# Optimization experiments

Measured on AMD Instinct MI355X. Metric: run time of the kernel, lower is better.

Reference implementation:

```python
import jax, jax.numpy as jnp
import numpy as np

B, T, S = 64, 128, 16
E = 512           # d2v input size
H = 512           # bi-LSTM output size (args.d2v_embed)
Hh = H // 2       # per-direction hidden
NL = 2            # num_layers
ED = 128          # args.embedding_dim
USERS, ARTS, PAD = 100000, 100000, 0


def setup_inputs() -> dict:
    key = jax.random.key(0)
    ks = jax.random.split(key, 32)
    p = 0.02
    inp = {}
    inp["x1"] = jax.random.normal(ks[0], (B, T, E), jnp.float32)
    inp["sample_d2v_embeds"] = jax.random.normal(ks[1], (B, T, S, H), jnp.float32)
    # LSTM params: layer-0 input E == layer-1 input H, so stackable. gate order i,f,g,o
    inp["lstm_Wih"] = jax.random.normal(ks[2], (NL, 2, 4 * Hh, E), jnp.float32) * p
    inp["lstm_Whh"] = jax.random.normal(ks[3], (NL, 2, 4 * Hh, Hh), jnp.float32) * p
    inp["lstm_bih"] = jax.random.normal(ks[4], (NL, 2, 4 * Hh), jnp.float32) * p
    inp["lstm_bhh"] = jax.random.normal(ks[5], (NL, 2, 4 * Hh), jnp.float32) * p
    inp["attn_W1"] = jax.random.normal(ks[6], (H, H), jnp.float32) * p
    inp["attn_b1"] = jax.random.normal(ks[7], (H,), jnp.float32) * p
    inp["attn_w2"] = jax.random.normal(ks[8], (H,), jnp.float32) * p
    inp["rnn_mlp_W"] = jax.random.normal(ks[9], (64, H), jnp.float32) * p
    inp["rnn_mlp_b"] = jax.random.normal(ks[10], (64,), jnp.float32) * p
    inp["user_table"] = jax.random.normal(ks[11], (USERS, ED), jnp.float32) * p
    inp["art_table"] = (jax.random.normal(ks[12], (ARTS, ED), jnp.float32) * p).at[PAD].set(0.0)
    inp["em_W1"] = jax.random.normal(ks[13], (128, ED), jnp.float32) * p
    inp["em_b1"] = jax.random.normal(ks[14], (128,), jnp.float32) * p
    inp["em_W2"] = jax.random.normal(ks[15], (64, 128), jnp.float32) * p
    inp["em_b2"] = jax.random.normal(ks[16], (64,), jnp.float32) * p
    inp["lm_W1"] = jax.random.normal(ks[17], (256, 128), jnp.float32) * p
    inp["lm_b1"] = jax.random.normal(ks[18], (256,), jnp.float32) * p
    inp["lm_W2"] = jax.random.normal(ks[19], (128, 256), jnp.float32) * p
    inp["lm_b2"] = jax.random.normal(ks[20], (128,), jnp.float32) * p
    inp["lm_W3"] = jax.random.normal(ks[21], (64, 128), jnp.float32) * p
    inp["lm_b3"] = jax.random.normal(ks[22], (64,), jnp.float32) * p
    inp["lm_W4"] = jax.random.normal(ks[23], (1, 64), jnp.float32) * p
    inp["lm_b4"] = jax.random.normal(ks[24], (1,), jnp.float32) * p
    inp["x2"] = 0  # unused '_' arg
    inp["cate"] = jax.random.randint(ks[25], (B, T), 0, 10)  # unused by forward
    lens = jax.random.randint(ks[26], (B,), 1, T + 1)
    inp["seq_lens"] = jnp.sort(lens)[::-1]  # pack requires descending
    inp["user_ids"] = jax.random.randint(ks[27], (B,), 0, USERS)
    inp["sample_ids"] = jax.random.randint(ks[28], (B, T, S), 0, ARTS)
    return inp


def _bilstm(x, lens, Wih, Whh, bih, bhh):
    # Packed bidirectional LSTM == padded LSTM with state updates masked to t < len.
    Bc, Tc, _ = x.shape
    tmask = jnp.arange(Tc)[None, :] < lens[:, None]       # [B,T]
    m_t = tmask.T[:, :, None]                             # [T,B,1]
    for l in range(NL):
        outs = []
        for d, rev in ((0, False), (1, True)):
            xg = jnp.einsum('bti,gi->tbg', x, Wih[l, d]) + bih[l, d]  # [T,B,4Hh]
            Whh_ld, bhh_ld = Whh[l, d], bhh[l, d]

            def step(carry, inp_t, Whh_ld=Whh_ld, bhh_ld=bhh_ld):
                h, c = carry
                xg_t, m = inp_t
                g = xg_t + h @ Whh_ld.T + bhh_ld
                i_, f_, g_, o_ = jnp.split(g, 4, axis=-1)
                c2 = jax.nn.sigmoid(f_) * c + jax.nn.sigmoid(i_) * jnp.tanh(g_)
                h2 = jax.nn.sigmoid(o_) * jnp.tanh(c2)
                h = jnp.where(m, h2, h)
                c = jnp.where(m, c2, c)
                return (h, c), h

            init = (jnp.zeros((Bc, Hh), x.dtype), jnp.zeros((Bc, Hh), x.dtype))
            _, hs = jax.lax.scan(step, init, (xg, m_t), reverse=rev)
            outs.append(jnp.transpose(hs, (1, 0, 2)))
        x = jnp.concatenate(outs, axis=-1)                # [B,T,H]
    return x, tmask


def reference(x1, sample_d2v_embeds, lstm_Wih, lstm_Whh, lstm_bih, lstm_bhh,
              attn_W1, attn_b1, attn_w2, rnn_mlp_W, rnn_mlp_b,
              user_table, art_table, em_W1, em_b1, em_W2, em_b2,
              lm_W1, lm_b1, lm_W2, lm_b2, lm_W3, lm_b3, lm_W4, lm_b4,
              x2, cate, seq_lens, user_ids, sample_ids):
    rnn, tmask = _bilstm(x1, seq_lens, lstm_Wih, lstm_Whh, lstm_bih, lstm_bhh)
    # per-key MLP attention score, causal softmax, weighted sum (the packed double loop)
    sc = jnp.einsum('bth,h->bt', jnp.tanh(jnp.einsum('bth,oh->bto', rnn, attn_W1) + attn_b1), attn_w2)
    causal = jnp.tril(jnp.ones((rnn.shape[1], rnn.shape[1]), bool))
    logits = jnp.where(causal[None, :, :], sc[:, None, :], jnp.float32(-1e30))
    a = jax.nn.softmax(logits, axis=-1)                   # [B,T(query),T(key)]
    ctx = jnp.einsum('bts,bsh->bth', a, rnn)
    ctx = jnp.where(tmask[:, :, None], ctx, 0.0)          # rnn_step zeros at padded t
    # embedding branch
    ue = user_table[user_ids]                             # [B,ED]
    se = art_table[sample_ids]                            # [B,T,S,ED]
    e = ue[:, None, None, :] * se
    e = jax.nn.relu(e @ em_W1.T + em_b1)
    e = jax.nn.relu(e @ em_W2.T + em_b2)                  # [B,T,S,64]
    # rnn branch
    r = ctx[:, :, None, :] * sample_d2v_embeds
    r = r @ rnn_mlp_W.T + rnn_mlp_b                       # [B,T,S,64]
    z = jnp.concatenate([e, r], axis=-1)                  # [B,T,S,128]
    z = jax.nn.relu(z @ lm_W1.T + lm_b1)
    z = jax.nn.relu(z @ lm_W2.T + lm_b2)
    z = jax.nn.relu(z @ lm_W3.T + lm_b3)
    z = jax.nn.sigmoid(z @ lm_W4.T + lm_b4)
    return jnp.squeeze(z, axis=-1)                        # [B,T,S]
```

## Files before the change

kernel.cpp:

```cpp
#include <hip/hip_runtime.h>
#include <cstddef>

namespace {

constexpr int T = 128;

typedef unsigned short u16;
typedef unsigned int u32;
typedef __attribute__((ext_vector_type(8))) short short8;
typedef __attribute__((ext_vector_type(4))) float f32x4;
typedef __attribute__((ext_vector_type(4))) int i32x4;

__device__ __forceinline__ u16 f2bf(float x) {
  u32 u = __float_as_uint(x);
  u = (u + 0x7FFFu + ((u >> 16) & 1u)) >> 16;
  return (u16)u;
}
__device__ __forceinline__ float bf2f(u16 v) {
  return __uint_as_float(((u32)v) << 16);
}
__device__ __forceinline__ float sigf(float x) {
  return __builtin_amdgcn_rcpf(1.f + __builtin_amdgcn_exp2f(-1.44269504f * x));
}
__device__ __forceinline__ float tanh2(float x) {
  return 1.f - 2.f * __builtin_amdgcn_rcpf(1.f + __builtin_amdgcn_exp2f(2.88539008f * x));
}
__device__ __forceinline__ void bar_lds() {
  asm volatile("s_waitcnt lgkmcnt(0)\n\ts_barrier" ::: "memory");
}

constexpr int O_WIH = 0;
constexpr int O_AW1 = 2097152;
constexpr int O_EM1 = 2359296;
constexpr int O_EM2 = 2375680;
constexpr int O_MLP = 2383872;
constexpr int O_LW1 = 2416640;
constexpr int O_LW2 = 2449408;
constexpr int O_LW3 = 2482176;
constexpr int N_WBF = 2490368;

__global__ __launch_bounds__(256)
void k_prep(const float* __restrict__ wih, const float* __restrict__ aw1,
            const float* __restrict__ e1, const float* __restrict__ e2,
            const float* __restrict__ mw, const float* __restrict__ l1,
            const float* __restrict__ l2, const float* __restrict__ l3,
            u16* __restrict__ wbf) {
  int i = blockIdx.x * 256 + threadIdx.x;
  if (i >= N_WBF) return;
  float v;
  if (i < O_AW1)      v = wih[i];
  else if (i < O_EM1) v = aw1[i - O_AW1];
  else if (i < O_EM2) v = e1[i - O_EM1];
  else if (i < O_MLP) v = e2[i - O_EM2];
  else if (i < O_LW1) v = mw[i - O_MLP];
  else if (i < O_LW2) v = l1[i - O_LW1];
  else if (i < O_LW3) v = l2[i - O_LW2];
  else                v = l3[i - O_LW3];
  wbf[i] = f2bf(v);
}

__global__ __launch_bounds__(256)
void k_prepw(const float* __restrict__ whh, signed char* __restrict__ wq) {
  int i = blockIdx.x * 256 + threadIdx.x;
  float v = whh[i] * 1016.f;
  v = fminf(fmaxf(v, -127.f), 127.f);
  wq[i] = (signed char)(int)rintf(v);
}

__global__ __launch_bounds__(256)
void k_xg_mfma(const float* __restrict__ X, const u16* __restrict__ Wbf,
               const float* __restrict__ bi, const float* __restrict__ bh,
               float* __restrict__ xg) {
  __shared__ __align__(16) u16 sx[32 * 520];
  int tid = threadIdx.x;
  int rowbase = blockIdx.x * 32;
  int nchunk = blockIdx.y;
  for (int idx = tid; idx < 4096; idx += 256) {
    int r = idx >> 7, k4 = idx & 127;
    float4 v = *(const float4*)(X + (size_t)(rowbase + r) * 512 + k4 * 4);
    u32* p = (u32*)(sx + r * 520 + k4 * 4);
    p[0] = (u32)f2bf(v.x) | ((u32)f2bf(v.y) << 16);
    p[1] = (u32)f2bf(v.z) | ((u32)f2bf(v.w) << 16);
  }
  __syncthreads();
  int w = tid >> 6, lane = tid & 63;
  int msub = w >> 1, nhalf = w & 1;
  int mbase = msub * 16;
  int nb0 = nchunk * 256 + nhalf * 128;
  f32x4 acc[8];
#pragma unroll
  for (int i = 0; i < 8; ++i) acc[i] = f32x4{0.f, 0.f, 0.f, 0.f};
  for (int kt = 0; kt < 16; ++kt) {
    short8 a = *(const short8*)(sx + (mbase + (lane & 15)) * 520 + kt * 32 + (lane >> 4) * 8);
#pragma unroll
    for (int nt = 0; nt < 8; ++nt) {
      short8 b = *(const short8*)(Wbf + (size_t)(nb0 + nt * 16 + (lane & 15)) * 512 +
                                  kt * 32 + (lane >> 4) * 8);
      acc[nt] = __builtin_amdgcn_mfma_f32_16x16x32_bf16(a, b, acc[nt], 0, 0, 0);
    }
  }
  int mr = mbase + (lane >> 4) * 4;
#pragma unroll
  for (int nt = 0; nt < 8; ++nt) {
    int n = nb0 + nt * 16 + (lane & 15);
    float bb = bi[n] + bh[n];
#pragma unroll
    for (int r = 0; r < 4; ++r)
      xg[(size_t)(rowbase + mr + r) * 2048 + n] = acc[nt][r] + bb;
  }
}

__global__ __launch_bounds__(512, 1)
void k_lstm6(const float* __restrict__ xg, const signed char* __restrict__ wq,
             const int* __restrict__ lens, float* __restrict__ out, int layer) {
  __shared__ __align__(16) signed char hq[2][16 * 272];
  const int d = blockIdx.x >> 2, bg = blockIdx.x & 3;
  const int tid = threadIdx.x;
  const int jc = tid >> 6, l = tid & 63, ln = l & 15, lk = l >> 4;
  const int mb = bg * 16;

  i32x4 Bq[4][2][4];
  const signed char* wbase = wq + (size_t)(layer * 2 + d) * 262144;
#pragma unroll
  for (int g = 0; g < 4; ++g)
#pragma unroll
    for (int js = 0; js < 2; ++js)
#pragma unroll
      for (int kc = 0; kc < 4; ++kc) {
        int n = g * 256 + jc * 32 + js * 16 + ln;
        Bq[g][js][kc] = *(const i32x4*)(wbase + (size_t)n * 256 + kc * 64 + lk * 16);
      }

  int mlen[4];
#pragma unroll
  for (int r = 0; r < 4; ++r) mlen[r] = lens[mb + lk * 4 + r];

  float cst[2][4], hst[2][4];
#pragma unroll
  for (int js = 0; js < 2; ++js)
#pragma unroll
    for (int r = 0; r < 4; ++r) { cst[js][r] = 0.f; hst[js][r] = 0.f; }

  const float DEQ = 1.f / (1016.f * 127.f);

  float xv[4][2][4];
  {
    int t0 = d ? 127 : 0;
#pragma unroll
    for (int g = 0; g < 4; ++g)
#pragma unroll
      for (int js = 0; js < 2; ++js)
#pragma unroll
        for (int r = 0; r < 4; ++r)
          xv[g][js][r] = xg[((size_t)(mb + lk * 4 + r) * 128 + t0) * 2048 +
                            d * 1024 + g * 256 + jc * 32 + js * 16 + ln];
  }

  for (int s = 0; s < 128; ++s) {
    const int t = d ? (127 - s) : s;

    float xvn[4][2][4];
    if (s < 127) {
      const int tn = d ? (127 - (s + 1)) : (s + 1);
#pragma unroll
      for (int g = 0; g < 4; ++g)
#pragma unroll
        for (int js = 0; js < 2; ++js)
#pragma unroll
          for (int r = 0; r < 4; ++r)
            xvn[g][js][r] = xg[((size_t)(mb + lk * 4 + r) * 128 + tn) * 2048 +
                               d * 1024 + g * 256 + jc * 32 + js * 16 + ln];
    }

    i32x4 acc[4][2];
#pragma unroll
    for (int g = 0; g < 4; ++g)
#pragma unroll
      for (int js = 0; js < 2; ++js) acc[g][js] = i32x4{0, 0, 0, 0};

    if (s > 0) {
      const signed char* hr = hq[(s & 1) ^ 1];
#pragma unroll
      for (int kc = 0; kc < 4; ++kc) {
        i32x4 a = *(const i32x4*)(hr + ln * 272 + kc * 64 + lk * 16);
#pragma unroll
        for (int g = 0; g < 4; ++g)
#pragma unroll
          for (int js = 0; js < 2; ++js)
            acc[g][js] = __builtin_amdgcn_mfma_i32_16x16x64_i8(a, Bq[g][js][kc],
                                                               acc[g][js], 0, 0, 0);
      }
    }

    signed char* hw = hq[s & 1];
#pragma unroll
    for (int js = 0; js < 2; ++js)
#pragma unroll
      for (int r = 0; r < 4; ++r) {
        float gi = (float)acc[0][js][r] * DEQ + xv[0][js][r];
        float gf = (float)acc[1][js][r] * DEQ + xv[1][js][r];
        float gg = (float)acc[2][js][r] * DEQ + xv[2][js][r];
        float go = (float)acc[3][js][r] * DEQ + xv[3][js][r];
        float c2 = sigf(gf) * cst[js][r] + sigf(gi) * tanh2(gg);
        float h2 = sigf(go) * tanh2(c2);
        const int m = lk * 4 + r;
        bool upd = t < mlen[r];
        cst[js][r] = upd ? c2 : cst[js][r];
        float hn = upd ? h2 : hst[js][r];
        hst[js][r] = hn;
        const int j = jc * 32 + js * 16 + ln;
        out[((size_t)(mb + m) * 128 + t) * 512 + d * 256 + j] = hn;
        hw[m * 272 + j] = (signed char)(int)rintf(hn * 127.f);
      }

    if (s < 127) {
#pragma unroll
      for (int g = 0; g < 4; ++g)
#pragma unroll
        for (int js = 0; js < 2; ++js)
#pragma unroll
          for (int r = 0; r < 4; ++r) xv[g][js][r] = xvn[g][js][r];
    }
    bar_lds();
  }
}

__global__ __launch_bounds__(256)
void k_attn(const float* __restrict__ rnn, const u16* __restrict__ W1bf,
            const float* __restrict__ b1, const float* __restrict__ w2,
            float* __restrict__ sc) {
  __shared__ __align__(16) u16 sx[32 * 520];
  __shared__ float sred[32];
  int tid = threadIdx.x;
  int rowbase = blockIdx.x * 32;
  for (int idx = tid; idx < 4096; idx += 256) {
    int r = idx >> 7, k4 = idx & 127;
    float4 v = *(const float4*)(rnn + (size_t)(rowbase + r) * 512 + k4 * 4);
    u32* p = (u32*)(sx + r * 520 + k4 * 4);
    p[0] = (u32)f2bf(v.x) | ((u32)f2bf(v.y) << 16);
    p[1] = (u32)f2bf(v.z) | ((u32)f2bf(v.w) << 16);
  }
  if (tid < 32) sred[tid] = 0.f;
  __syncthreads();
  int w = tid >> 6, lane = tid & 63;
  int msub = w >> 1, nhalf = w & 1;
  int mbase = msub * 16;
  float psum[4] = {0.f, 0.f, 0.f, 0.f};
  for (int ng = 0; ng < 4; ++ng) {
    f32x4 acc[4];
#pragma unroll
    for (int i = 0; i < 4; ++i) acc[i] = f32x4{0.f, 0.f, 0.f, 0.f};
    for (int kt = 0; kt < 16; ++kt) {
      short8 a = *(const short8*)(sx + (mbase + (lane & 15)) * 520 + kt * 32 + (lane >> 4) * 8);
#pragma unroll
      for (int nt = 0; nt < 4; ++nt) {
        int nrow = nhalf * 256 + ng * 64 + nt * 16 + (lane & 15);
        short8 b = *(const short8*)(W1bf + (size_t)nrow * 512 + kt * 32 + (lane >> 4) * 8);
        acc[nt] = __builtin_amdgcn_mfma_f32_16x16x32_bf16(a, b, acc[nt], 0, 0, 0);
      }
    }
#pragma unroll
    for (int nt = 0; nt < 4; ++nt) {
      int n = nhalf * 256 + ng * 64 + nt * 16 + (lane & 15);
      float wn = w2[n], bn = b1[n];
#pragma unroll
      for (int r = 0; r < 4; ++r) psum[r] += wn * tanh2(acc[nt][r] + bn);
    }
  }
#pragma unroll
  for (int off = 8; off >= 1; off >>= 1)
#pragma unroll
    for (int r = 0; r < 4; ++r) psum[r] += __shfl_xor(psum[r], off);
  if ((lane & 15) == 0) {
#pragma unroll
    for (int r = 0; r < 4; ++r)
      atomicAdd(&sred[msub * 16 + (lane >> 4) * 4 + r], psum[r]);
  }
  __syncthreads();
  if (tid < 32) sc[rowbase + tid] = sred[tid];
}

__global__ __launch_bounds__(128)
void k_ctx(const float* __restrict__ sc, const float* __restrict__ rnn,
           const int* __restrict__ lens, float* __restrict__ ctx) {
  int b = blockIdx.x;
  int h = blockIdx.y * 128 + threadIdx.x;
  __shared__ float ex[T];
  ex[threadIdx.x] = expf(sc[b * T + threadIdx.x]);
  __syncthreads();
  int len = lens[b];
  float acc = 0.f, den = 0.f;
  for (int t = 0; t < T; ++t) {
    float wv = ex[t];
    den += wv;
    acc += wv * rnn[((size_t)b * T + t) * 512 + h];
    ctx[((size_t)b * T + t) * 512 + h] = (t < len) ? (acc / den) : 0.f;
  }
}

template <int NT, int KT, bool RELU>
__device__ __forceinline__ void stage_mfma(const u16* __restrict__ Wbf,
                                           const float* __restrict__ bias,
                                           const u16* A, int lda,
                                           u16* O, int ldo, int nofs,
                                           int lane, int msub, int nhalf) {
  f32x4 acc[NT];
#pragma unroll
  for (int i = 0; i < NT; ++i) acc[i] = f32x4{0.f, 0.f, 0.f, 0.f};
  int mbase = msub * 16;
  int nb0 = nhalf * (NT * 16);
#pragma unroll
  for (int kt = 0; kt < KT; ++kt) {
    short8 a = *(const short8*)(A + (mbase + (lane & 15)) * lda + kt * 32 + (lane >> 4) * 8);
#pragma unroll
    for (int nt = 0; nt < NT; ++nt) {
      short8 b = *(const short8*)(Wbf + (size_t)(nb0 + nt * 16 + (lane & 15)) * (KT * 32) +
                                  kt * 32 + (lane >> 4) * 8);
      acc[nt] = __builtin_amdgcn_mfma_f32_16x16x32_bf16(a, b, acc[nt], 0, 0, 0);
    }
  }
  int mr = mbase + (lane >> 4) * 4;
#pragma unroll
  for (int nt = 0; nt < NT; ++nt) {
    int nl = nb0 + nt * 16 + (lane & 15);
    float bv = bias[nl];
#pragma unroll
    for (int r = 0; r < 4; ++r) {
      float v = acc[nt][r] + bv;
      if (RELU) v = fmaxf(v, 0.f);
      O[(mr + r) * ldo + nofs + nl] = f2bf(v);
    }
  }
}

__global__ __launch_bounds__(256)
void k_sample(const float* __restrict__ ctx, const float* __restrict__ d2v,
              const float* __restrict__ user_table, const float* __restrict__ art_table,
              const int* __restrict__ user_ids, const int* __restrict__ sample_ids,
              const u16* __restrict__ wbf,
              const float* __restrict__ em_b1, const float* __restrict__ em_b2,
              const float* __restrict__ mlp_b,
              const float* __restrict__ lm_b1, const float* __restrict__ lm_b2,
              const float* __restrict__ lm_b3,
              const float* __restrict__ lm_W4, const float* __restrict__ lm_b4,
              float* __restrict__ out) {
  __shared__ __align__(16) u16 bufA[32 * 264];
  __shared__ __align__(16) u16 bufB[32 * 264];
  __shared__ __align__(16) u16 bufC[32 * 136];
  __shared__ float sred[32];
  int tid = threadIdx.x, lane = tid & 63, w = tid >> 6;
  int msub = w >> 1, nhalf = w & 1;
  int mbase = msub * 16;
  int rowbase = blockIdx.x * 32;

  if (tid < 32) sred[tid] = 0.f;

  float4 uu[4], aa[4];
#pragma unroll
  for (int it = 0; it < 4; ++it) {
    int idx = it * 256 + tid;
    int r = idx >> 5, k4 = idx & 31;
    int m = rowbase + r;
    int sid = sample_ids[m];
    int uid = user_ids[m >> 11];
    uu[it] = *(const float4*)(user_table + (size_t)uid * 128 + k4 * 4);
    aa[it] = *(const float4*)(art_table + (size_t)sid * 128 + k4 * 4);
  }
  float4 dd0[8];
#pragma unroll
  for (int it = 0; it < 8; ++it) {
    int idx = it * 256 + tid;
    int r = idx >> 6, k4 = idx & 63;
    int m = rowbase + r;
    dd0[it] = *(const float4*)(d2v + (size_t)m * 512 + k4 * 4);
  }

#pragma unroll
  for (int it = 0; it < 4; ++it) {
    int idx = it * 256 + tid;
    int r = idx >> 5, k4 = idx & 31;
    float4 u = uu[it], a = aa[it];
    u32* p = (u32*)(bufA + r * 264 + k4 * 4);
    p[0] = (u32)f2bf(u.x * a.x) | ((u32)f2bf(u.y * a.y) << 16);
    p[1] = (u32)f2bf(u.z * a.z) | ((u32)f2bf(u.w * a.w) << 16);
  }
  bar_lds();
  stage_mfma<4, 4, true>(wbf + O_EM1, em_b1, bufA, 264, bufB, 264, 0, lane, msub, nhalf);
  bar_lds();
  stage_mfma<2, 4, true>(wbf + O_EM2, em_b2, bufB, 264, bufC, 136, 0, lane, msub, nhalf);
  float4 dd1[8];
#pragma unroll
  for (int it = 0; it < 8; ++it) {
    int idx = it * 256 + tid;
    int r = idx >> 6, k4 = idx & 63;
    int m = rowbase + r;
    dd1[it] = *(const float4*)(d2v + (size_t)m * 512 + 256 + k4 * 4);
  }
#pragma unroll
  for (int it = 0; it < 8; ++it) {
    int idx = it * 256 + tid;
    int r = idx >> 6, k4 = idx & 63;
    int m = rowbase + r;
    int bt = m >> 4;
    float4 cx = *(const float4*)(ctx + (size_t)bt * 512 + k4 * 4);
    float4 dv = dd0[it];
    u32* p = (u32*)(bufA + r * 264 + k4 * 4);
    p[0] = (u32)f2bf(cx.x * dv.x) | ((u32)f2bf(cx.y * dv.y) << 16);
    p[1] = (u32)f2bf(cx.z * dv.z) | ((u32)f2bf(cx.w * dv.w) << 16);
  }
  bar_lds();

  f32x4 racc[2];
  racc[0] = f32x4{0.f, 0.f, 0.f, 0.f};
  racc[1] = f32x4{0.f, 0.f, 0.f, 0.f};
  for (int kc = 0; kc < 2; ++kc) {
#pragma unroll
    for (int kt = 0; kt < 8; ++kt) {
      short8 a = *(const short8*)(bufA + (mbase + (lane & 15)) * 264 + kt * 32 + (lane >> 4) * 8);
#pragma unroll
      for (int nt = 0; nt < 2; ++nt) {
        int n = nhalf * 32 + nt * 16 + (lane & 15);
        short8 b = *(const short8*)(wbf + O_MLP + (size_t)n * 512 + kc * 256 +
                                    kt * 32 + (lane >> 4) * 8);
        racc[nt] = __builtin_amdgcn_mfma_f32_16x16x32_bf16(a, b, racc[nt], 0, 0, 0);
      }
    }
    bar_lds();
    if (kc == 0) {
#pragma unroll
      for (int it = 0; it < 8; ++it) {
        int idx = it * 256 + tid;
        int r = idx >> 6, k4 = idx & 63;
        int m = rowbase + r;
        int bt = m >> 4;
        float4 cx = *(const float4*)(ctx + (size_t)bt * 512 + 256 + k4 * 4);
        float4 dv = dd1[it];
        u32* p = (u32*)(bufA + r * 264 + k4 * 4);
        p[0] = (u32)f2bf(cx.x * dv.x) | ((u32)f2bf(cx.y * dv.y) << 16);
        p[1] = (u32)f2bf(cx.z * dv.z) | ((u32)f2bf(cx.w * dv.w) << 16);
      }
      bar_lds();
    }
  }
  {
    int mr = mbase + (lane >> 4) * 4;
#pragma unroll
    for (int nt = 0; nt < 2; ++nt) {
      int nl = nhalf * 32 + nt * 16 + (lane & 15);
      float bv = mlp_b[nl];
#pragma unroll
      for (int r = 0; r < 4; ++r)
        bufC[(mr + r) * 136 + 64 + nl] = f2bf(racc[nt][r] + bv);
    }
  }
  bar_lds();
  stage_mfma<8, 4, true>(wbf + O_LW1, lm_b1, bufC, 136, bufB, 264, 0, lane, msub, nhalf);
  bar_lds();
  stage_mfma<4, 8, true>(wbf + O_LW2, lm_b2, bufB, 264, bufA, 264, 0, lane, msub, nhalf);
  bar_lds();

  {
    f32x4 acc[2];
    acc[0] = f32x4{0.f, 0.f, 0.f, 0.f};
    acc[1] = f32x4{0.f, 0.f, 0.f, 0.f};
#pragma unroll
    for (int kt = 0; kt < 4; ++kt) {
      short8 a = *(const short8*)(bufA + (mbase + (lane & 15)) * 264 + kt * 32 + (lane >> 4) * 8);
#pragma unroll
      for (int nt = 0; nt < 2; ++nt) {
        int n = nhalf * 32 + nt * 16 + (lane & 15);
        short8 b = *(const short8*)(wbf + O_LW3 + (size_t)n * 128 +
                                    kt * 32 + (lane >> 4) * 8);
        acc[nt] = __builtin_amdgcn_mfma_f32_16x16x32_bf16(a, b, acc[nt], 0, 0, 0);
      }
    }
    float psum[4] = {0.f, 0.f, 0.f, 0.f};
#pragma unroll
    for (int nt = 0; nt < 2; ++nt) {
      int nl = nhalf * 32 + nt * 16 + (lane & 15);
      float bv = lm_b3[nl], w4 = lm_W4[nl];
#pragma unroll
      for (int r = 0; r < 4; ++r) psum[r] += w4 * fmaxf(acc[nt][r] + bv, 0.f);
    }
#pragma unroll
    for (int off = 8; off >= 1; off >>= 1)
#pragma unroll
      for (int r = 0; r < 4; ++r) psum[r] += __shfl_xor(psum[r], off);
    if ((lane & 15) == 0) {
#pragma unroll
      for (int r = 0; r < 4; ++r)
        atomicAdd(&sred[mbase + (lane >> 4) * 4 + r], psum[r]);
    }
  }
  bar_lds();
  if (tid < 32) out[rowbase + tid] = sigf(sred[tid] + lm_b4[0]);
}

}

extern "C" void kernel_launch(void* const* d_in, const int* in_sizes, int n_in,
                              void* d_out, int out_size, void* d_ws, size_t ws_size,
                              hipStream_t stream) {
  const float* x1   = (const float*)d_in[0];
  const float* d2v  = (const float*)d_in[1];
  const float* Wih  = (const float*)d_in[2];
  const float* Whh  = (const float*)d_in[3];
  const float* bih  = (const float*)d_in[4];
  const float* bhh  = (const float*)d_in[5];
  const float* aW1  = (const float*)d_in[6];
  const float* ab1  = (const float*)d_in[7];
  const float* aw2  = (const float*)d_in[8];
  const float* mlpW = (const float*)d_in[9];
  const float* mlpb = (const float*)d_in[10];
  const float* utab = (const float*)d_in[11];
  const float* atab = (const float*)d_in[12];
  const float* emW1 = (const float*)d_in[13];
  const float* emb1 = (const float*)d_in[14];
  const float* emW2 = (const float*)d_in[15];
  const float* emb2 = (const float*)d_in[16];
  const float* lmW1 = (const float*)d_in[17];
  const float* lmb1 = (const float*)d_in[18];
  const float* lmW2 = (const float*)d_in[19];
  const float* lmb2 = (const float*)d_in[20];
  const float* lmW3 = (const float*)d_in[21];
  const float* lmb3 = (const float*)d_in[22];
  const float* lmW4 = (const float*)d_in[23];
  const float* lmb4 = (const float*)d_in[24];
  const int* lens   = (const int*)d_in[27];
  const int* uids   = (const int*)d_in[28];
  const int* sids   = (const int*)d_in[29];
  float* out = (float*)d_out;

  float* ws = (float*)d_ws;
  signed char* WQ = (signed char*)ws;
  float* SC  = ws + 262144;
  u16* WBF = (u16*)(ws + 270336);
  float* XG  = ws + 1515520;
  float* R0  = ws + 18292736;
  float* R1  = ws + 22487040;
  float* CTX = ws + 18292736;

  k_prep<<<(N_WBF + 255) / 256, 256, 0, stream>>>(Wih, aW1, emW1, emW2, mlpW,
                                                  lmW1, lmW2, lmW3, WBF);
  k_prepw<<<4096, 256, 0, stream>>>(Whh, WQ);
  k_xg_mfma<<<dim3(256, 8), 256, 0, stream>>>(x1, WBF + O_WIH, bih, bhh, XG);
  k_lstm6<<<8, 512, 0, stream>>>(XG, WQ, lens, R0, 0);
  k_xg_mfma<<<dim3(256, 8), 256, 0, stream>>>(R0, WBF + O_WIH + 1048576,
                                              bih + 2048, bhh + 2048, XG);
  k_lstm6<<<8, 512, 0, stream>>>(XG, WQ, lens, R1, 1);
  k_attn<<<256, 256, 0, stream>>>(R1, WBF + O_AW1, ab1, aw2, SC);
  k_ctx<<<dim3(64, 4), 128, 0, stream>>>(SC, R1, lens, CTX);
  k_sample<<<4096, 256, 0, stream>>>(CTX, d2v, utab, atab, uids, sids, WBF,
                                     emb1, emb2, mlpb, lmb1, lmb2, lmb3,
                                     lmW4, lmb4, out);
}
```

Before: 1.378 ms.

## Double LSTM recurrence block to 1024 threads, one column tile per wave

The recurrent LSTM kernel now runs 16 waves per block instead of 8, so each wave owns 16 hidden columns rather than 32. That halves the per-wave MFMA chain and the gate math on the serial critical path, and halves the register footprint of the resident int8 weights. The software prefetch of the next timestep's input-gate values is removed, so those loads now happen inside each step. This may expose global-load latency on every step, and the barrier now has to synchronize more waves.

```diff
diff --git a/kernel.cpp b/kernel.cpp
--- a/kernel.cpp
+++ b/kernel.cpp
@@ -110,7 +110,7 @@
   }
 }
 
-__global__ __launch_bounds__(512, 1)
+__global__ __launch_bounds__(1024, 1)
 void k_lstm6(const float* __restrict__ xg, const signed char* __restrict__ wq,
              const int* __restrict__ lens, float* __restrict__ out, int layer) {
   __shared__ __align__(16) signed char hq[2][16 * 272];
@@ -118,65 +118,42 @@
   const int tid = threadIdx.x;
   const int jc = tid >> 6, l = tid & 63, ln = l & 15, lk = l >> 4;
   const int mb = bg * 16;
-
-  i32x4 Bq[4][2][4];
+  const int j = jc * 16 + ln;
+
+  i32x4 Bq[4][4];
   const signed char* wbase = wq + (size_t)(layer * 2 + d) * 262144;
 #pragma unroll
   for (int g = 0; g < 4; ++g)
 #pragma unroll
-    for (int js = 0; js < 2; ++js)
-#pragma unroll
-      for (int kc = 0; kc < 4; ++kc) {
-        int n = g * 256 + jc * 32 + js * 16 + ln;
-        Bq[g][js][kc] = *(const i32x4*)(wbase + (size_t)n * 256 + kc * 64 + lk * 16);
-      }
+    for (int kc = 0; kc < 4; ++kc) {
+      int n = g * 256 + j;
+      Bq[g][kc] = *(const i32x4*)(wbase + (size_t)n * 256 + kc * 64 + lk * 16);
+    }
 
   int mlen[4];
 #pragma unroll
   for (int r = 0; r < 4; ++r) mlen[r] = lens[mb + lk * 4 + r];
 
-  float cst[2][4], hst[2][4];
-#pragma unroll
-  for (int js = 0; js < 2; ++js)
-#pragma unroll
-    for (int r = 0; r < 4; ++r) { cst[js][r] = 0.f; hst[js][r] = 0.f; }
+  float cst[4], hst[4];
+#pragma unroll
+  for (int r = 0; r < 4; ++r) { cst[r] = 0.f; hst[r] = 0.f; }
 
   const float DEQ = 1.f / (1016.f * 127.f);
-
-  float xv[4][2][4];
-  {
-    int t0 = d ? 127 : 0;
-#pragma unroll
-    for (int g = 0; g < 4; ++g)
-#pragma unroll
-      for (int js = 0; js < 2; ++js)
-#pragma unroll
-        for (int r = 0; r < 4; ++r)
-          xv[g][js][r] = xg[((size_t)(mb + lk * 4 + r) * 128 + t0) * 2048 +
-                            d * 1024 + g * 256 + jc * 32 + js * 16 + ln];
-  }
 
   for (int s = 0; s < 128; ++s) {
     const int t = d ? (127 - s) : s;
 
-    float xvn[4][2][4];
-    if (s < 127) {
-      const int tn = d ? (127 - (s + 1)) : (s + 1);
-#pragma unroll
-      for (int g = 0; g < 4; ++g)
-#pragma unroll
-        for (int js = 0; js < 2; ++js)
-#pragma unroll
-          for (int r = 0; r < 4; ++r)
-            xvn[g][js][r] = xg[((size_t)(mb + lk * 4 + r) * 128 + tn) * 2048 +
-                               d * 1024 + g * 256 + jc * 32 + js * 16 + ln];
-    }
-
-    i32x4 acc[4][2];
+    float xv[4][4];
 #pragma unroll
     for (int g = 0; g < 4; ++g)
 #pragma unroll
-      for (int js = 0; js < 2; ++js) acc[g][js] = i32x4{0, 0, 0, 0};
+      for (int r = 0; r < 4; ++r)
+        xv[g][r] = xg[((size_t)(mb + lk * 4 + r) * 128 + t) * 2048 +
+                      d * 1024 + g * 256 + j];
+
+    i32x4 acc[4];
+#pragma unroll
+    for (int g = 0; g < 4; ++g) acc[g] = i32x4{0, 0, 0, 0};
 
     if (s > 0) {
       const signed char* hr = hq[(s & 1) ^ 1];
@@ -185,41 +162,26 @@
         i32x4 a = *(const i32x4*)(hr + ln * 272 + kc * 64 + lk * 16);
 #pragma unroll
         for (int g = 0; g < 4; ++g)
-#pragma unroll
-          for (int js = 0; js < 2; ++js)
-            acc[g][js] = __builtin_amdgcn_mfma_i32_16x16x64_i8(a, Bq[g][js][kc],
-                                                               acc[g][js], 0, 0, 0);
+          acc[g] = __builtin_amdgcn_mfma_i32_16x16x64_i8(a, Bq[g][kc], acc[g], 0, 0, 0);
       }
     }
 
     signed char* hw = hq[s & 1];
 #pragma unroll
-    for (int js = 0; js < 2; ++js)
-#pragma unroll
-      for (int r = 0; r < 4; ++r) {
-        float gi = (float)acc[0][js][r] * DEQ + xv[0][js][r];
-        float gf = (float)acc[1][js][r] * DEQ + xv[1][js][r];
-        float gg = (float)acc[2][js][r] * DEQ + xv[2][js][r];
-        float go = (float)acc[3][js][r] * DEQ + xv[3][js][r];
-        float c2 = sigf(gf) * cst[js][r] + sigf(gi) * tanh2(gg);
-        float h2 = sigf(go) * tanh2(c2);
-        const int m = lk * 4 + r;
-        bool upd = t < mlen[r];
-        cst[js][r] = upd ? c2 : cst[js][r];
-        float hn = upd ? h2 : hst[js][r];
-        hst[js][r] = hn;
-        const int j = jc * 32 + js * 16 + ln;
-        out[((size_t)(mb + m) * 128 + t) * 512 + d * 256 + j] = hn;
-        hw[m * 272 + j] = (signed char)(int)rintf(hn * 127.f);
-      }
-
-    if (s < 127) {
-#pragma unroll
-      for (int g = 0; g < 4; ++g)
-#pragma unroll
-        for (int js = 0; js < 2; ++js)
-#pragma unroll
-          for (int r = 0; r < 4; ++r) xv[g][js][r] = xvn[g][js][r];
+    for (int r = 0; r < 4; ++r) {
+      float gi = (float)acc[0][r] * DEQ + xv[0][r];
+      float gf = (float)acc[1][r] * DEQ + xv[1][r];
+      float gg = (float)acc[2][r] * DEQ + xv[2][r];
+      float go = (float)acc[3][r] * DEQ + xv[3][r];
+      float c2 = sigf(gf) * cst[r] + sigf(gi) * tanh2(gg);
+      float h2 = sigf(go) * tanh2(c2);
+      const int m = lk * 4 + r;
+      bool upd = t < mlen[r];
+      cst[r] = upd ? c2 : cst[r];
+      float hn = upd ? h2 : hst[r];
+      hst[r] = hn;
+      out[((size_t)(mb + m) * 128 + t) * 512 + d * 256 + j] = hn;
+      hw[m * 272 + j] = (signed char)(int)rintf(hn * 127.f);
     }
     bar_lds();
   }
@@ -544,10 +506,10 @@
                                                   lmW1, lmW2, lmW3, WBF);
   k_prepw<<<4096, 256, 0, stream>>>(Whh, WQ);
   k_xg_mfma<<<dim3(256, 8), 256, 0, stream>>>(x1, WBF + O_WIH, bih, bhh, XG);
-  k_lstm6<<<8, 512, 0, stream>>>(XG, WQ, lens, R0, 0);
+  k_lstm6<<<8, 1024, 0, stream>>>(XG, WQ, lens, R0, 0);
   k_xg_mfma<<<dim3(256, 8), 256, 0, stream>>>(R0, WBF + O_WIH + 1048576,
                                               bih + 2048, bhh + 2048, XG);
-  k_lstm6<<<8, 512, 0, stream>>>(XG, WQ, lens, R1, 1);
+  k_lstm6<<<8, 1024, 0, stream>>>(XG, WQ, lens, R1, 1);
   k_attn<<<256, 256, 0, stream>>>(R1, WBF + O_AW1, ab1, aw2, SC);
   k_ctx<<<dim3(64, 4), 128, 0, stream>>>(SC, R1, lens, CTX);
   k_sample<<<4096, 256, 0, stream>>>(CTX, d2v, utab, atab, uids, sids, WBF,
```

Measured after the change: 1.648 ms. 1.2x slower.

## Overlap embedding-branch MLP with latency-bound LSTM by adding extra blocks

Applied to the files above, without the earlier changes.

The embedding branch (user*article gather, two bf16 MFMA layers) moves out of the sample kernel into 2048 extra blocks of the first LSTM launch. These blocks run on idle CUs while the 8 serial LSTM blocks step through time, and they write a bf16 intermediate that the sample kernel then reads back. The LSTM loop also drops its one-step-ahead prefetch of the input-gate values and loads them inline each step, which may expose global load latency on the serial critical path. The sample kernel becomes lighter, but it adds an extra 128-byte-per-row round trip through global memory.

```diff
diff --git a/kernel.cpp b/kernel.cpp
--- a/kernel.cpp
+++ b/kernel.cpp
@@ -7,6 +7,7 @@
 
 typedef unsigned short u16;
 typedef unsigned int u32;
+typedef unsigned long long u64;
 typedef __attribute__((ext_vector_type(8))) short short8;
 typedef __attribute__((ext_vector_type(4))) float f32x4;
 typedef __attribute__((ext_vector_type(4))) int i32x4;
@@ -110,12 +111,107 @@
   }
 }
 
+template <int NT, int KT, bool RELU>
+__device__ __forceinline__ void stage_mfma(const u16* __restrict__ Wbf,
+                                           const float* __restrict__ bias,
+                                           const u16* A, int lda,
+                                           u16* O, int ldo, int nofs,
+                                           int lane, int msub, int nhalf) {
+  f32x4 acc[NT];
+#pragma unroll
+  for (int i = 0; i < NT; ++i) acc[i] = f32x4{0.f, 0.f, 0.f, 0.f};
+  int mbase = msub * 16;
+  int nb0 = nhalf * (NT * 16);
+#pragma unroll
+  for (int kt = 0; kt < KT; ++kt) {
+    short8 a = *(const short8*)(A + (mbase + (lane & 15)) * lda + kt * 32 + (lane >> 4) * 8);
+#pragma unroll
+    for (int nt = 0; nt < NT; ++nt) {
+      short8 b = *(const short8*)(Wbf + (size_t)(nb0 + nt * 16 + (lane & 15)) * (KT * 32) +
+                                  kt * 32 + (lane >> 4) * 8);
+      acc[nt] = __builtin_amdgcn_mfma_f32_16x16x32_bf16(a, b, acc[nt], 0, 0, 0);
+    }
+  }
+  int mr = mbase + (lane >> 4) * 4;
+#pragma unroll
+  for (int nt = 0; nt < NT; ++nt) {
+    int nl = nb0 + nt * 16 + (lane & 15);
+    float bv = bias[nl];
+#pragma unroll
+    for (int r = 0; r < 4; ++r) {
+      float v = acc[nt][r] + bv;
+      if (RELU) v = fmaxf(v, 0.f);
+      O[(mr + r) * ldo + nofs + nl] = f2bf(v);
+    }
+  }
+}
+
 __global__ __launch_bounds__(512, 1)
 void k_lstm6(const float* __restrict__ xg, const signed char* __restrict__ wq,
-             const int* __restrict__ lens, float* __restrict__ out, int layer) {
+             const int* __restrict__ lens, float* __restrict__ out, int layer,
+             const float* __restrict__ utab, const float* __restrict__ atab,
+             const int* __restrict__ uids, const int* __restrict__ sids,
+             const u16* __restrict__ wbf, const float* __restrict__ em_b1,
+             const float* __restrict__ em_b2, u16* __restrict__ ez) {
   __shared__ __align__(16) signed char hq[2][16 * 272];
+  __shared__ __align__(16) u16 ebufA[2 * 32 * 136];
+  __shared__ __align__(16) u16 ebufB[2 * 32 * 136];
+  const int tid = threadIdx.x;
+
+  if (blockIdx.x >= 8) {
+    const int half = tid >> 8;
+    const int t = tid & 255;
+    const int lane = t & 63, wv = t >> 6;
+    const int msub = wv >> 1, nhalf = wv & 1;
+    const int rowbase = ((int)blockIdx.x - 8) * 64 + half * 32;
+    u16* eA = ebufA + half * 4352;
+    u16* eB = ebufB + half * 4352;
+#pragma unroll
+    for (int it = 0; it < 4; ++it) {
+      int idx = it * 256 + t;
+      int r = idx >> 5, k4 = idx & 31;
+      int m = rowbase + r;
+      int sid = sids[m];
+      int uid = uids[m >> 11];
+      float4 u = *(const float4*)(utab + (size_t)uid * 128 + k4 * 4);
+      float4 a = *(const float4*)(atab + (size_t)sid * 128 + k4 * 4);
+      u32* p = (u32*)(eA + r * 136 + k4 * 4);
+      p[0] = (u32)f2bf(u.x * a.x) | ((u32)f2bf(u.y * a.y) << 16);
+      p[1] = (u32)f2bf(u.z * a.z) | ((u32)f2bf(u.w * a.w) << 16);
+    }
+    bar_lds();
+    stage_mfma<4, 4, true>(wbf + O_EM1, em_b1, eA, 136, eB, 136, 0, lane, msub, nhalf);
+    bar_lds();
+    {
+      f32x4 acc[2];
+      acc[0] = f32x4{0.f, 0.f, 0.f, 0.f};
+      acc[1] = f32x4{0.f, 0.f, 0.f, 0.f};
+#pragma unroll
+      for (int kt = 0; kt < 4; ++kt) {
+        short8 a = *(const short8*)(eB + (msub * 16 + (lane & 15)) * 136 +
+                                    kt * 32 + (lane >> 4) * 8);
+#pragma unroll
+        for (int nt = 0; nt < 2; ++nt) {
+          int n = nhalf * 32 + nt * 16 + (lane & 15);
+          short8 b = *(const short8*)(wbf + O_EM2 + (size_t)n * 128 +
+                                      kt * 32 + (lane >> 4) * 8);
+          acc[nt] = __builtin_amdgcn_mfma_f32_16x16x32_bf16(a, b, acc[nt], 0, 0, 0);
+        }
+      }
+      int mr = msub * 16 + (lane >> 4) * 4;
+#pragma unroll
+      for (int nt = 0; nt < 2; ++nt) {
+        int n = nhalf * 32 + nt * 16 + (lane & 15);
+        float bv = em_b2[n];
+#pragma unroll
+        for (int r = 0; r < 4; ++r)
+          ez[(size_t)(rowbase + mr + r) * 64 + n] = f2bf(fmaxf(acc[nt][r] + bv, 0.f));
+      }
+    }
+    return;
+  }
+
   const int d = blockIdx.x >> 2, bg = blockIdx.x & 3;
-  const int tid = threadIdx.x;
   const int jc = tid >> 6, l = tid & 63, ln = l & 15, lk = l >> 4;
   const int mb = bg * 16;
 
@@ -143,34 +239,18 @@
 
   const float DEQ = 1.f / (1016.f * 127.f);
 
-  float xv[4][2][4];
-  {
-    int t0 = d ? 127 : 0;
-#pragma unroll
-    for (int g = 0; g < 4; ++g)
-#pragma unroll
-      for (int js = 0; js < 2; ++js)
-#pragma unroll
-        for (int r = 0; r < 4; ++r)
-          xv[g][js][r] = xg[((size_t)(mb + lk * 4 + r) * 128 + t0) * 2048 +
-                            d * 1024 + g * 256 + jc * 32 + js * 16 + ln];
-  }
-
   for (int s = 0; s < 128; ++s) {
     const int t = d ? (127 - s) : s;
 
-    float xvn[4][2][4];
-    if (s < 127) {
-      const int tn = d ? (127 - (s + 1)) : (s + 1);
-#pragma unroll
-      for (int g = 0; g < 4; ++g)
-#pragma unroll
-        for (int js = 0; js < 2; ++js)
-#pragma unroll
-          for (int r = 0; r < 4; ++r)
-            xvn[g][js][r] = xg[((size_t)(mb + lk * 4 + r) * 128 + tn) * 2048 +
-                               d * 1024 + g * 256 + jc * 32 + js * 16 + ln];
-    }
+    float xv[4][2][4];
+#pragma unroll
+    for (int g = 0; g < 4; ++g)
+#pragma unroll
+      for (int js = 0; js < 2; ++js)
+#pragma unroll
+        for (int r = 0; r < 4; ++r)
+          xv[g][js][r] = xg[((size_t)(mb + lk * 4 + r) * 128 + t) * 2048 +
+                            d * 1024 + g * 256 + jc * 32 + js * 16 + ln];
 
     i32x4 acc[4][2];
 #pragma unroll
@@ -212,15 +292,6 @@
         out[((size_t)(mb + m) * 128 + t) * 512 + d * 256 + j] = hn;
         hw[m * 272 + j] = (signed char)(int)rintf(hn * 127.f);
       }
-
-    if (s < 127) {
-#pragma unroll
-      for (int g = 0; g < 4; ++g)
-#pragma unroll
-        for (int js = 0; js < 2; ++js)
-#pragma unroll
-          for (int r = 0; r < 4; ++r) xv[g][js][r] = xvn[g][js][r];
-    }
     bar_lds();
   }
 }
@@ -298,48 +369,10 @@
   }
 }
 
-template <int NT, int KT, bool RELU>
-__device__ __forceinline__ void stage_mfma(const u16* __restrict__ Wbf,
-                                           const float* __restrict__ bias,
-                                           const u16* A, int lda,
-                                           u16* O, int ldo, int nofs,
-                                           int lane, int msub, int nhalf) {
-  f32x4 acc[NT];
-#pragma unroll
-  for (int i = 0; i < NT; ++i) acc[i] = f32x4{0.f, 0.f, 0.f, 0.f};
-  int mbase = msub * 16;
-  int nb0 = nhalf * (NT * 16);
-#pragma unroll
-  for (int kt = 0; kt < KT; ++kt) {
-    short8 a = *(const short8*)(A + (mbase + (lane & 15)) * lda + kt * 32 + (lane >> 4) * 8);
-#pragma unroll
-    for (int nt = 0; nt < NT; ++nt) {
-      short8 b = *(const short8*)(Wbf + (size_t)(nb0 + nt * 16 + (lane & 15)) * (KT * 32) +
-                                  kt * 32 + (lane >> 4) * 8);
-      acc[nt] = __builtin_amdgcn_mfma_f32_16x16x32_bf16(a, b, acc[nt], 0, 0, 0);
-    }
-  }
-  int mr = mbase + (lane >> 4) * 4;
-#pragma unroll
-  for (int nt = 0; nt < NT; ++nt) {
-    int nl = nb0 + nt * 16 + (lane & 15);
-    float bv = bias[nl];
-#pragma unroll
-    for (int r = 0; r < 4; ++r) {
-      float v = acc[nt][r] + bv;
-      if (RELU) v = fmaxf(v, 0.f);
-      O[(mr + r) * ldo + nofs + nl] = f2bf(v);
-    }
-  }
-}
-
 __global__ __launch_bounds__(256)
 void k_sample(const float* __restrict__ ctx, const float* __restrict__ d2v,
-              const float* __restrict__ user_table, const float* __restrict__ art_table,
-              const int* __restrict__ user_ids, const int* __restrict__ sample_ids,
-              const u16* __restrict__ wbf,
-              const float* __restrict__ em_b1, const float* __restrict__ em_b2,
-              const float* __restrict__ mlp_b,
+              const u16* __restrict__ ez,
+              const u16* __restrict__ wbf, const float* __restrict__ mlp_b,
               const float* __restrict__ lm_b1, const float* __restrict__ lm_b2,
               const float* __restrict__ lm_b3,
               const float* __restrict__ lm_W4, const float* __restrict__ lm_b4,
@@ -355,18 +388,13 @@
 
   if (tid < 32) sred[tid] = 0.f;
 
-  float4 uu[4], aa[4];
-#pragma unroll
-  for (int it = 0; it < 4; ++it) {
-    int idx = it * 256 + tid;
-    int r = idx >> 5, k4 = idx & 31;
-    int m = rowbase + r;
-    int sid = sample_ids[m];
-    int uid = user_ids[m >> 11];
-    uu[it] = *(const float4*)(user_table + (size_t)uid * 128 + k4 * 4);
-    aa[it] = *(const float4*)(art_table + (size_t)sid * 128 + k4 * 4);
-  }
-  float4 dd0[8];
+  for (int idx = tid; idx < 512; idx += 256) {
+    int r = idx >> 4, q = idx & 15;
+    *(u64*)(bufC + r * 136 + q * 4) =
+        *(const u64*)(ez + (size_t)(rowbase + r) * 64 + q * 4);
+  }
+
+  float4 dd0[8], dd1[8];
 #pragma unroll
   for (int it = 0; it < 8; ++it) {
     int idx = it * 256 + tid;
@@ -374,21 +402,6 @@
     int m = rowbase + r;
     dd0[it] = *(const float4*)(d2v + (size_t)m * 512 + k4 * 4);
   }
-
-#pragma unroll
-  for (int it = 0; it < 4; ++it) {
-    int idx = it * 256 + tid;
-    int r = idx >> 5, k4 = idx & 31;
-    float4 u = uu[it], a = aa[it];
-    u32* p = (u32*)(bufA + r * 264 + k4 * 4);
-    p[0] = (u32)f2bf(u.x * a.x) | ((u32)f2bf(u.y * a.y) << 16);
-    p[1] = (u32)f2bf(u.z * a.z) | ((u32)f2bf(u.w * a.w) << 16);
-  }
-  bar_lds();
-  stage_mfma<4, 4, true>(wbf + O_EM1, em_b1, bufA, 264, bufB, 264, 0, lane, msub, nhalf);
-  bar_lds();
-  stage_mfma<2, 4, true>(wbf + O_EM2, em_b2, bufB, 264, bufC, 136, 0, lane, msub, nhalf);
-  float4 dd1[8];
 #pragma unroll
   for (int it = 0; it < 8; ++it) {
     int idx = it * 256 + tid;
@@ -396,6 +409,7 @@
     int m = rowbase + r;
     dd1[it] = *(const float4*)(d2v + (size_t)m * 512 + 256 + k4 * 4);
   }
+
 #pragma unroll
   for (int it = 0; it < 8; ++it) {
     int idx = it * 256 + tid;
@@ -538,19 +552,23 @@
   float* XG  = ws + 1515520;
   float* R0  = ws + 18292736;
   float* R1  = ws + 22487040;
+  u16* EZ  = (u16*)(ws + 26681344);
   float* CTX = ws + 18292736;
 
   k_prep<<<(N_WBF + 255) / 256, 256, 0, stream>>>(Wih, aW1, emW1, emW2, mlpW,
                                                   lmW1, lmW2, lmW3, WBF);
   k_prepw<<<4096, 256, 0, stream>>>(Whh, WQ);
   k_xg_mfma<<<dim3(256, 8), 256, 0, stream>>>(x1, WBF + O_WIH, bih, bhh, XG);
-  k_lstm6<<<8, 512, 0, stream>>>(XG, WQ, lens, R0, 0);
+  k_lstm6<<<8 + 2048, 512, 0, stream>>>(XG, WQ, lens, R0, 0,
+                                        utab, atab, uids, sids,
+                                        WBF, emb1, emb2, EZ);
   k_xg_mfma<<<dim3(256, 8), 256, 0, stream>>>(R0, WBF + O_WIH + 1048576,
                                               bih + 2048, bhh + 2048, XG);
-  k_lstm6<<<8, 512, 0, stream>>>(XG, WQ, lens, R1, 1);
+  k_lstm6<<<8, 512, 0, stream>>>(XG, WQ, lens, R1, 1,
+                                 utab, atab, uids, sids,
+                                 WBF, emb1, emb2, EZ);
   k_attn<<<256, 256, 0, stream>>>(R1, WBF + O_AW1, ab1, aw2, SC);
   k_ctx<<<dim3(64, 4), 128, 0, stream>>>(SC, R1, lens, CTX);
-  k_sample<<<4096, 256, 0, stream>>>(CTX, d2v, utab, atab, uids, sids, WBF,
-                                     emb1, emb2, mlpb, lmb1, lmb2, lmb3,
-                                     lmW4, lmb4, out);
-}
+  k_sample<<<4096, 256, 0, stream>>>(CTX, d2v, EZ, WBF, mlpb,
+                                     lmb1, lmb2, lmb3, lmW4, lmb4, out);
+}
```

Result: faster. 1.176 ms (-14.7%).
